# Kernel optimization log

Measured on AMD Instinct MI355X. Metric: run time of the kernel, lower is better.

The kernel has to match this reference:

```python
import jax, jax.numpy as jnp
import numpy as np

B, S, HID = 2, 2048, 2048
NH, NKV, DH = 32, 8, 64
WIN = 1024


def rotate_half(x):
    x1, x2 = x[..., : x.shape[-1] // 2], x[..., x.shape[-1] // 2:]
    return jnp.concatenate((-x2, x1), axis=-1)


def setup_inputs() -> dict:
    key = jax.random.key(0)
    ks = jax.random.split(key, 8)
    hidden_states = jax.random.normal(ks[0], (B, S, HID), dtype=jnp.float32)
    # real RoPE tables: [B, S, DH]
    inv_freq = 1.0 / (10000.0 ** (np.arange(0, DH, 2, dtype=np.float32) / DH))
    ang = np.arange(S, dtype=np.float32)[:, None] * inv_freq[None, :]  # [S, DH/2]
    emb = np.concatenate([ang, ang], axis=-1)  # [S, DH]
    cos = jnp.broadcast_to(jnp.asarray(np.cos(emb)), (B, S, DH))
    sin = jnp.broadcast_to(jnp.asarray(np.sin(emb)), (B, S, DH))
    sc = 0.02
    Wq = jax.random.normal(ks[1], (NH * DH, HID), dtype=jnp.float32) * sc
    Wk = jax.random.normal(ks[2], (NKV * DH, HID), dtype=jnp.float32) * sc
    Wv = jax.random.normal(ks[3], (NKV * DH, HID), dtype=jnp.float32) * sc
    Wo = jax.random.normal(ks[4], (HID, NH * DH), dtype=jnp.float32) * sc
    return {"hidden_states": hidden_states, "cos": cos, "sin": sin,
            "Wq": Wq, "Wk": Wk, "Wv": Wv, "Wo": Wo}


def sliding_window_mask(q_len, k_len, dtype):
    half = WIN // 2
    qi = jnp.arange(q_len)[:, None]
    ki = jnp.arange(k_len)[None, :]
    last = jnp.clip(qi + half, None, k_len - 1)
    first = jnp.clip(qi - half, 0, None)
    visible = (ki >= first) & (ki <= last)
    minv = jnp.finfo(dtype).min
    return jnp.where(visible, jnp.array(0.0, dtype), jnp.array(minv, dtype))  # [q_len, k_len]


def reference(hidden_states, cos, sin, Wq, Wk, Wv, Wo):
    b, s, _ = hidden_states.shape
    scale = DH ** -0.5
    q = (hidden_states @ Wq.T).reshape(b, s, NH, DH).transpose(0, 2, 1, 3)   # [B,NH,S,DH]
    k = (hidden_states @ Wk.T).reshape(b, s, NKV, DH).transpose(0, 2, 1, 3)  # [B,NKV,S,DH]
    v = (hidden_states @ Wv.T).reshape(b, s, NKV, DH).transpose(0, 2, 1, 3)
    c, sn = cos[:, None, :, :], sin[:, None, :, :]  # broadcast over heads
    q = q * c + rotate_half(q) * sn
    k = k * c + rotate_half(k) * sn
    groups = NH // NKV
    k = jnp.repeat(k, groups, axis=1)  # [B,NH,S,DH]
    v = jnp.repeat(v, groups, axis=1)
    mask = sliding_window_mask(s, s, hidden_states.dtype)  # [S,S]
    scores = jnp.einsum("bhqd,bhkd->bhqk", q, k) * scale + mask  # dense quadratic bias add
    attn = jax.nn.softmax(scores, axis=-1)
    out = jnp.einsum("bhqk,bhkd->bhqd", attn, v)
    out = out.transpose(0, 2, 1, 3).reshape(b, s, NH * DH)
    return out @ Wo.T
```

## Files before the change

### kernel.cpp

```cpp
#include <hip/hip_runtime.h>
#include <hip/hip_bf16.h>
#include <stdint.h>
#include <stddef.h>

#define S_LEN 2048
#define HIDDEN 2048
#define NHEAD 32
#define NKVH 8
#define DHEAD 64
#define BATCH 2
#define HALFW 512
#define QSCALE 0.18033688011112042f

typedef __attribute__((ext_vector_type(4))) float f32x4;
typedef __attribute__((ext_vector_type(8))) short short8;
typedef __attribute__((ext_vector_type(4))) short short4v;
typedef __attribute__((ext_vector_type(2))) unsigned int u32x2;

__device__ __forceinline__ unsigned short f2bf(float f) {
  unsigned u = __builtin_bit_cast(unsigned, f);
  u += 0x7fffu + ((u >> 16) & 1u);
  return (unsigned short)(u >> 16);
}
__device__ __forceinline__ float bf2f(unsigned short h) {
  unsigned u = ((unsigned)h) << 16;
  return __builtin_bit_cast(float, u);
}
__device__ __forceinline__ unsigned cvt_pk_bf16(float lo, float hi) {
  unsigned r;
  asm("v_cvt_pk_bf16_f32 %0, %1, %2" : "=v"(r) : "v"(lo), "v"(hi));
  return r;
}

__global__ void k_cvt5(const float* __restrict__ s0, const float* __restrict__ s1,
                       const float* __restrict__ s2, const float* __restrict__ s3,
                       const float* __restrict__ s4,
                       unsigned short* __restrict__ d0, unsigned short* __restrict__ d1,
                       unsigned short* __restrict__ d2, unsigned short* __restrict__ d3,
                       unsigned short* __restrict__ d4) {
  int i = blockIdx.x * blockDim.x + threadIdx.x;
#pragma unroll 1
  for (int it = 0; it < 9; ++it, i += 524288) {
    const float* src;
    unsigned short* dst;
    int base;
    if (i < 2097152)      { src = s0; dst = d0; base = 0; }
    else if (i < 3145728) { src = s1; dst = d1; base = 2097152; }
    else if (i < 3407872) { src = s2; dst = d2; base = 3145728; }
    else if (i < 3670016) { src = s3; dst = d3; base = 3407872; }
    else                  { src = s4; dst = d4; base = 3670016; }
    int j = i - base;
    float4 v = reinterpret_cast<const float4*>(src)[j];
    short4v o;
    o[0] = (short)f2bf(v.x);
    o[1] = (short)f2bf(v.y);
    o[2] = (short)f2bf(v.z);
    o[3] = (short)f2bf(v.w);
    reinterpret_cast<short4v*>(dst)[j] = o;
  }
}

template <int MODE>
__global__ __launch_bounds__(256) void k_gemm_bt(const unsigned short* __restrict__ A,
                                                 const unsigned short* __restrict__ Bw,
                                                 void* __restrict__ Cout,
                                                 const float* __restrict__ cosb,
                                                 const float* __restrict__ sinb,
                                                 unsigned short* __restrict__ Qr,
                                                 unsigned short* __restrict__ Kr,
                                                 unsigned short* __restrict__ Vrow,
                                                 int M, int N, int K) {
  __shared__ unsigned short As[128][32];
  __shared__ unsigned short Bs[128][32];
  const int tid = threadIdx.x;
  const int wid = tid >> 6;
  const int lane = tid & 63;
  const int l15 = lane & 15;
  const int lhi = lane >> 4;
  const int bm = blockIdx.y * 128;
  const int bn = blockIdx.x * 128;
  const int wm = (wid >> 1) * 64;
  const int wn = (wid & 1) * 64;
  f32x4 acc[4][4] = {};

  for (int k0 = 0; k0 < K; k0 += 32) {
#pragma unroll
    for (int i = 0; i < 2; ++i) {
      int u = i * 256 + tid;
      int row = u >> 2, c8 = u & 3;
      const unsigned short* ga = A + (size_t)(bm + row) * K + k0 + c8 * 8;
      const unsigned short* gb = Bw + (size_t)(bn + row) * K + k0 + c8 * 8;
      __builtin_amdgcn_global_load_lds(
          (const __attribute__((address_space(1))) unsigned int*)(const void*)ga,
          (__attribute__((address_space(3))) unsigned int*)(void*)((char*)&As[0][0] + i * 4096 + wid * 1024),
          16, 0, 0);
      __builtin_amdgcn_global_load_lds(
          (const __attribute__((address_space(1))) unsigned int*)(const void*)gb,
          (__attribute__((address_space(3))) unsigned int*)(void*)((char*)&Bs[0][0] + i * 4096 + wid * 1024),
          16, 0, 0);
    }
    __syncthreads();

    short8 af[4], bfr[4];
#pragma unroll
    for (int m = 0; m < 4; ++m)
      af[m] = *reinterpret_cast<const short8*>(&As[wm + m * 16 + l15][lhi * 8]);
#pragma unroll
    for (int n = 0; n < 4; ++n)
      bfr[n] = *reinterpret_cast<const short8*>(&Bs[wn + n * 16 + l15][lhi * 8]);
#pragma unroll
    for (int m = 0; m < 4; ++m)
#pragma unroll
      for (int n = 0; n < 4; ++n)
        acc[m][n] = __builtin_amdgcn_mfma_f32_16x16x32_bf16(af[m], bfr[n], acc[m][n], 0, 0, 0);
    __syncthreads();
  }

  if (MODE == 1) {
#pragma unroll
    for (int m = 0; m < 4; ++m) {
#pragma unroll
      for (int r = 0; r < 4; ++r) {
        int row = bm + wm + m * 16 + lhi * 4 + r;
#pragma unroll
        for (int n = 0; n < 4; ++n) {
          int col = bn + wn + n * 16 + l15;
          ((float*)Cout)[(size_t)row * N + col] = acc[m][n][r];
        }
      }
    }
  } else {
    const int hc = (bn + wn) >> 6;
#pragma unroll
    for (int m = 0; m < 4; ++m) {
#pragma unroll
      for (int r = 0; r < 4; ++r) {
        int row = bm + wm + m * 16 + lhi * 4 + r;
        int b = row >> 11, s = row & 2047;
        if (hc < 40) {
#pragma unroll
          for (int n = 0; n < 2; ++n) {
            int d = n * 16 + l15;
            float c = cosb[(size_t)row * DHEAD + d];
            float sn = sinb[(size_t)row * DHEAD + d];
            float x1 = acc[m][n][r];
            float x2 = acc[m][n + 2][r];
            float o1 = x1 * c - x2 * sn;
            float o2 = x2 * c + x1 * sn;
            if (hc < 32) {
              size_t o = ((size_t)(b * NHEAD + hc) * S_LEN + s) * DHEAD + d;
              Qr[o] = f2bf(o1 * QSCALE);
              Qr[o + 32] = f2bf(o2 * QSCALE);
            } else {
              size_t o = ((size_t)(b * NKVH + (hc - 32)) * S_LEN + s) * DHEAD + d;
              Kr[o] = f2bf(o1);
              Kr[o + 32] = f2bf(o2);
            }
          }
        } else {
#pragma unroll
          for (int n = 0; n < 4; ++n) {
            int d = n * 16 + l15;
            size_t o = ((size_t)(b * NKVH + (hc - 40)) * S_LEN + s) * DHEAD + d;
            Vrow[o] = f2bf(acc[m][n][r]);
          }
        }
      }
    }
  }
}

__global__ void k_vt(const unsigned short* __restrict__ Vrow, unsigned short* __restrict__ Vt) {
  __shared__ unsigned short t[64][68];
  int s0 = blockIdx.x * 64;
  int g = blockIdx.y;
  int tid = threadIdx.x;
#pragma unroll
  for (int it = 0; it < 4; ++it) {
    int u = it * 256 + tid;
    int srow = u >> 4, c4 = u & 15;
    short4v v = *reinterpret_cast<const short4v*>(
        &Vrow[((size_t)g * S_LEN + s0 + srow) * DHEAD + c4 * 4]);
    *reinterpret_cast<short4v*>(&t[srow][c4 * 4]) = v;
  }
  __syncthreads();
#pragma unroll
  for (int it = 0; it < 4; ++it) {
    int u = it * 256 + tid;
    int d = u >> 4, s4 = u & 15;
    short4v v;
#pragma unroll
    for (int j = 0; j < 4; ++j) v[j] = t[s4 * 4 + j][d];
    *reinterpret_cast<short4v*>(
        &Vt[((size_t)g * DHEAD + d) * S_LEN + s0 + s4 * 4]) = v;
  }
}

__global__ __launch_bounds__(256, 4) void k_attn(const unsigned short* __restrict__ Qr,
                                                 const unsigned short* __restrict__ Kr,
                                                 const unsigned short* __restrict__ Vt,
                                                 unsigned short* __restrict__ AO) {
  __shared__ unsigned short Ks[2][64][64];
  __shared__ unsigned short Vs[2][64][64];
  __shared__ unsigned short Pl[4][16][64];

  const int tid = threadIdx.x, w = tid >> 6, lane = tid & 63;
  const int l15 = lane & 15, lhi = lane >> 4;

  int p = blockIdx.x;
  int L = (p & 7) * 256 + (p >> 3);
  int g = L >> 7;
  int b = g >> 3, hk = g & 7;
  int r_ = L & 127;
  int h = hk * 4 + (r_ >> 5);
  int q0b = (r_ & 31) * 64;
  const int qw = q0b + w * 16;

  const unsigned short* Qh = Qr + (size_t)(b * NHEAD + h) * S_LEN * DHEAD;
  const unsigned short* Kh = Kr + (size_t)(b * NKVH + hk) * S_LEN * DHEAD;
  const unsigned short* Vh = Vt + (size_t)(b * NKVH + hk) * DHEAD * S_LEN;

  short8 qf[2];
#pragma unroll
  for (int c = 0; c < 2; ++c)
    qf[c] = *reinterpret_cast<const short8*>(&Qh[(size_t)(qw + l15) * DHEAD + c * 32 + lhi * 8]);

  f32x4 o[4] = {};
  float den = 0.f;
  const int q = qw + l15;
  const int kvisLo = q - HALFW, kvisHi = q + HALFW;

  char* plbase = (char*)&Pl[w][0][0];
  const int swzp = (l15 & 7) << 4;

  int klo = q0b - HALFW; if (klo < 0) klo = 0;
  klo &= ~63;
  int khi = q0b + 63 + HALFW; if (khi > S_LEN - 1) khi = S_LEN - 1;
  const int nt = ((khi + 1 - klo) + 63) >> 6;

  auto stage = [&](int bufidx, int kbb) {
#pragma unroll
    for (int i = 0; i < 2; ++i) {
      int u = i * 256 + tid;
      int row = u >> 3, c16 = u & 7;
      int sc = c16 ^ (row & 7);
      __builtin_amdgcn_global_load_lds(
          (const __attribute__((address_space(1))) unsigned int*)(const void*)
              (Kh + (size_t)(kbb + row) * DHEAD + sc * 8),
          (__attribute__((address_space(3))) unsigned int*)(void*)
              ((char*)&Ks[bufidx][0][0] + u * 16),
          16, 0, 0);
      __builtin_amdgcn_global_load_lds(
          (const __attribute__((address_space(1))) unsigned int*)(const void*)
              (Vh + (size_t)row * S_LEN + kbb + sc * 8),
          (__attribute__((address_space(3))) unsigned int*)(void*)
              ((char*)&Vs[bufidx][0][0] + u * 16),
          16, 0, 0);
    }
  };

  int cur = 0;
  stage(0, klo);
  __syncthreads();

  for (int t = 0; t < nt; ++t) {
    const int kb = klo + t * 64;
    if (t + 1 < nt) stage(cur ^ 1, kb + 64);

    f32x4 sacc[4] = {};
    __builtin_amdgcn_s_setprio(1);
#pragma unroll
    for (int hh = 0; hh < 4; ++hh) {
      int kr = hh * 16 + l15;
      const char* kbase = (const char*)&Ks[cur][0][0] + kr * 128;
      short8 kf0 = *reinterpret_cast<const short8*>(kbase + ((lhi ^ (kr & 7)) * 16));
      short8 kf1 = *reinterpret_cast<const short8*>(kbase + (((4 + lhi) ^ (kr & 7)) * 16));
      sacc[hh] = __builtin_amdgcn_mfma_f32_16x16x32_bf16(kf0, qf[0], sacc[hh], 0, 0, 0);
      sacc[hh] = __builtin_amdgcn_mfma_f32_16x16x32_bf16(kf1, qf[1], sacc[hh], 0, 0, 0);
    }
    __builtin_amdgcn_s_setprio(0);

    const bool inter = (kb >= qw + 15 - HALFW) && (kb + 63 <= qw + HALFW);
    if (inter) {
#pragma unroll
      for (int hh = 0; hh < 4; ++hh) {
        float p0 = __builtin_amdgcn_exp2f(sacc[hh][0]);
        float p1 = __builtin_amdgcn_exp2f(sacc[hh][1]);
        float p2 = __builtin_amdgcn_exp2f(sacc[hh][2]);
        float p3 = __builtin_amdgcn_exp2f(sacc[hh][3]);
        den += (p0 + p1) + (p2 + p3);
        u32x2 pw;
        pw[0] = cvt_pk_bf16(p0, p1);
        pw[1] = cvt_pk_bf16(p2, p3);
        *(u32x2*)(plbase + ((l15 * 128 + hh * 32 + lhi * 8) ^ swzp)) = pw;
      }
    } else {
#pragma unroll
      for (int hh = 0; hh < 4; ++hh) {
        float pp[4];
#pragma unroll
        for (int r = 0; r < 4; ++r) {
          int key = kb + hh * 16 + lhi * 4 + r;
          bool vis = (key >= kvisLo) && (key <= kvisHi);
          pp[r] = vis ? __builtin_amdgcn_exp2f(sacc[hh][r]) : 0.0f;
        }
        den += (pp[0] + pp[1]) + (pp[2] + pp[3]);
        u32x2 pw;
        pw[0] = cvt_pk_bf16(pp[0], pp[1]);
        pw[1] = cvt_pk_bf16(pp[2], pp[3]);
        *(u32x2*)(plbase + ((l15 * 128 + hh * 32 + lhi * 8) ^ swzp)) = pw;
      }
    }
    asm volatile("s_waitcnt lgkmcnt(0)" ::: "memory");
    __builtin_amdgcn_sched_barrier(0);

    short8 pf0 = *reinterpret_cast<const short8*>(plbase + ((l15 * 128 + lhi * 16) ^ swzp));
    short8 pf1 = *reinterpret_cast<const short8*>(plbase + ((l15 * 128 + 64 + lhi * 16) ^ swzp));
    __builtin_amdgcn_s_setprio(1);
#pragma unroll
    for (int c = 0; c < 4; ++c) {
      int d = c * 16 + l15;
      const char* vbase = (const char*)&Vs[cur][0][0] + d * 128;
      short8 vf0 = *reinterpret_cast<const short8*>(vbase + ((lhi ^ (d & 7)) * 16));
      short8 vf1 = *reinterpret_cast<const short8*>(vbase + (((4 + lhi) ^ (d & 7)) * 16));
      o[c] = __builtin_amdgcn_mfma_f32_16x16x32_bf16(pf0, vf0, o[c], 0, 0, 0);
      o[c] = __builtin_amdgcn_mfma_f32_16x16x32_bf16(pf1, vf1, o[c], 0, 0, 0);
    }
    __builtin_amdgcn_s_setprio(0);

    __syncthreads();
    cur ^= 1;
  }

  den += __shfl_xor(den, 16);
  den += __shfl_xor(den, 32);

#pragma unroll
  for (int r = 0; r < 4; ++r) {
    int qo = qw + lhi * 4 + r;
    float dr = __shfl(den, lhi * 4 + r, 64);
    float dinv = 1.0f / dr;
#pragma unroll
    for (int c = 0; c < 4; ++c)
      AO[(size_t)(b * S_LEN + qo) * HIDDEN + h * DHEAD + c * 16 + l15] = f2bf(o[c][r] * dinv);
  }
}

extern "C" void kernel_launch(void* const* d_in, const int* in_sizes, int n_in,
                              void* d_out, int out_size, void* d_ws, size_t ws_size,
                              hipStream_t stream) {
  const float* hs   = (const float*)d_in[0];
  const float* cosb = (const float*)d_in[1];
  const float* sinb = (const float*)d_in[2];
  const float* Wq   = (const float*)d_in[3];
  const float* Wk   = (const float*)d_in[4];
  const float* Wv   = (const float*)d_in[5];
  const float* Wo   = (const float*)d_in[6];

  char* ws = (char*)d_ws;
  unsigned short* Xbf  = (unsigned short*)(ws);
  unsigned short* Wqkv = (unsigned short*)(ws + 16777216);
  unsigned short* Vt   = (unsigned short*)(ws + 29360128);
  unsigned short* AO   = (unsigned short*)(ws + 33554432);
  unsigned short* Wob  = (unsigned short*)(ws + 54525952);

  unsigned short* Qr   = (unsigned short*)d_out;
  unsigned short* Kr   = Qr + (size_t)BATCH * NKVH * S_LEN * DHEAD * 4;
  unsigned short* Vrow = Kr + (size_t)BATCH * NKVH * S_LEN * DHEAD;

  k_cvt5<<<2048, 256, 0, stream>>>(hs, Wq, Wk, Wv, Wo,
                                   Xbf, Wqkv, Wqkv + 4194304, Wqkv + 5242880, Wob);

  k_gemm_bt<2><<<dim3(3072 / 128, 4096 / 128), 256, 0, stream>>>(
      Xbf, Wqkv, nullptr, cosb, sinb, Qr, Kr, Vrow, 4096, 3072, 2048);

  k_vt<<<dim3(S_LEN / 64, BATCH * NKVH), 256, 0, stream>>>(Vrow, Vt);

  k_attn<<<BATCH * NHEAD * (S_LEN / 64), 256, 0, stream>>>(Qr, Kr, Vt, AO);

  k_gemm_bt<1><<<dim3(2048 / 128, 4096 / 128), 256, 0, stream>>>(
      AO, Wob, d_out, nullptr, nullptr, nullptr, nullptr, nullptr, 4096, 2048, 2048);
}
```

Measured before the change: 215.3 us.

## Double GEMM K-tile to 64 and use conflict-free permuted LDS layout

The projection GEMM now stages a 64-wide K slice per iteration instead of 32, halving the number of barrier pairs and loop iterations. Shared-memory tiles are reorganised into a permuted layout where each 16-byte chunk's row and column index are remapped so that the direct global-to-LDS loads and the MFMA fragment reads hit distinct banks. This aims to cut LDS bank conflicts and synchronisation overhead, at the cost of doubled LDS usage per block, which may reduce occupancy.

```diff
diff --git a/kernel.cpp b/kernel.cpp
--- a/kernel.cpp
+++ b/kernel.cpp
@@ -70,8 +70,8 @@
                                                  unsigned short* __restrict__ Kr,
                                                  unsigned short* __restrict__ Vrow,
                                                  int M, int N, int K) {
-  __shared__ unsigned short As[128][32];
-  __shared__ unsigned short Bs[128][32];
+  __shared__ unsigned short As[8192];
+  __shared__ unsigned short Bs[8192];
   const int tid = threadIdx.x;
   const int wid = tid >> 6;
   const int lane = tid & 63;
@@ -83,36 +83,50 @@
   const int wn = (wid & 1) * 64;
   f32x4 acc[4][4] = {};
 
-  for (int k0 = 0; k0 < K; k0 += 32) {
-#pragma unroll
-    for (int i = 0; i < 2; ++i) {
+  int srow[4], sc16[4];
+#pragma unroll
+  for (int i = 0; i < 4; ++i) {
+    int u = i * 256 + tid;
+    srow[i] = (u & 7) | ((u >> 6) << 3);
+    sc16[i] = (u >> 3) & 7;
+  }
+
+  const int rdoff = (l15 & 7) * 16 + (l15 >> 3) * 1024 + lhi * 128;
+  const char* aL = (const char*)As + rdoff + (wm >> 6) * 8192;
+  const char* bL = (const char*)Bs + rdoff + (wn >> 6) * 8192;
+
+  for (int k0 = 0; k0 < K; k0 += 64) {
+#pragma unroll
+    for (int i = 0; i < 4; ++i) {
       int u = i * 256 + tid;
-      int row = u >> 2, c8 = u & 3;
-      const unsigned short* ga = A + (size_t)(bm + row) * K + k0 + c8 * 8;
-      const unsigned short* gb = Bw + (size_t)(bn + row) * K + k0 + c8 * 8;
+      const unsigned short* ga = A + (size_t)(bm + srow[i]) * K + k0 + sc16[i] * 8;
+      const unsigned short* gb = Bw + (size_t)(bn + srow[i]) * K + k0 + sc16[i] * 8;
       __builtin_amdgcn_global_load_lds(
           (const __attribute__((address_space(1))) unsigned int*)(const void*)ga,
-          (__attribute__((address_space(3))) unsigned int*)(void*)((char*)&As[0][0] + i * 4096 + wid * 1024),
+          (__attribute__((address_space(3))) unsigned int*)(void*)((char*)As + u * 16),
           16, 0, 0);
       __builtin_amdgcn_global_load_lds(
           (const __attribute__((address_space(1))) unsigned int*)(const void*)gb,
-          (__attribute__((address_space(3))) unsigned int*)(void*)((char*)&Bs[0][0] + i * 4096 + wid * 1024),
+          (__attribute__((address_space(3))) unsigned int*)(void*)((char*)Bs + u * 16),
           16, 0, 0);
     }
     __syncthreads();
 
-    short8 af[4], bfr[4];
-#pragma unroll
-    for (int m = 0; m < 4; ++m)
-      af[m] = *reinterpret_cast<const short8*>(&As[wm + m * 16 + l15][lhi * 8]);
-#pragma unroll
-    for (int n = 0; n < 4; ++n)
-      bfr[n] = *reinterpret_cast<const short8*>(&Bs[wn + n * 16 + l15][lhi * 8]);
-#pragma unroll
-    for (int m = 0; m < 4; ++m)
+#pragma unroll
+    for (int kk = 0; kk < 2; ++kk) {
+      short8 af[4], bfr[4];
+#pragma unroll
+      for (int m = 0; m < 4; ++m)
+        af[m] = *reinterpret_cast<const short8*>(aL + m * 2048 + kk * 512);
 #pragma unroll
       for (int n = 0; n < 4; ++n)
-        acc[m][n] = __builtin_amdgcn_mfma_f32_16x16x32_bf16(af[m], bfr[n], acc[m][n], 0, 0, 0);
+        bfr[n] = *reinterpret_cast<const short8*>(bL + n * 2048 + kk * 512);
+#pragma unroll
+      for (int m = 0; m < 4; ++m)
+#pragma unroll
+        for (int n = 0; n < 4; ++n)
+          acc[m][n] = __builtin_amdgcn_mfma_f32_16x16x32_bf16(af[m], bfr[n], acc[m][n], 0, 0, 0);
+    }
     __syncthreads();
   }
 
```

Result: slower. 267.9 us (+24.4%).
